# Optimization experiments

Hardware: AMD Instinct MI355X
Metric: run time of the kernel (lower is better)

## Reference

```python
import jax, jax.numpy as jnp
import numpy as np

CHUNK = 64          # config.memory_chunk_size
MAX_LR = 0.2        # config.max_memory_lr
MIN_DECAY = 0.5     # config.min_memory_decay
MAX_NORM = 30.0     # config.memory_max_norm
NORM_EPS = 1e-5     # config.norm_eps (F.normalize eps)


def setup_inputs() -> dict:
    key = jax.random.key(0)
    k0, k1 = jax.random.split(key)
    B, S, d_in, d_out = 8, 8192, 384, 384
    x = jax.random.normal(k0, (B, S, d_in), dtype=jnp.float32)
    # xavier_uniform with gain=0.1
    bound = 0.1 * float(np.sqrt(6.0 / (d_in + d_out)))
    M_init = jax.random.uniform(k1, (d_out, d_in), minval=-bound, maxval=bound, dtype=jnp.float32)
    eta_raw = jnp.asarray(np.log(0.08 / 0.92), jnp.float32)    # inv_sigmoid(memory_lr_init)
    alpha_raw = jnp.asarray(np.log(0.85 / 0.15), jnp.float32)  # inv_sigmoid(memory_decay_init)
    gate_w = jnp.zeros((1, d_in), jnp.float32)                 # nn.init.zeros_
    gate_b = jnp.full((1,), 2.0, jnp.float32)                  # nn.init.constant_(2.0)
    return {"x": x, "M_init": M_init, "eta_raw": eta_raw, "alpha_raw": alpha_raw,
            "gate_w": gate_w, "gate_b": gate_b}


def reference(x, M_init, eta_raw, alpha_raw, gate_w, gate_b):
    B, S, d_in = x.shape
    d_out = M_init.shape[0]
    eta = jax.nn.sigmoid(eta_raw) * MAX_LR
    alpha = MIN_DECAY + jax.nn.sigmoid(alpha_raw) * (1.0 - MIN_DECAY)

    n_chunks = S // CHUNK  # S chosen divisible by CHUNK => chunk_scale == 1.0
    xc = x.reshape(B, n_chunks, CHUNK, d_in).transpose(1, 0, 2, 3)  # [n,B,C,d_in]
    M0 = jnp.broadcast_to(M_init[None], (B, d_out, d_in)).astype(x.dtype)

    def step(M, chunk):
        # retrieve: queries @ M^T -> [B,C,d_out]
        out = jnp.einsum('bcd,bod->bco', chunk, M)
        # normalize keys (F.normalize: x / max(||x||, eps))
        norms = jnp.linalg.norm(chunk, axis=-1, keepdims=True)
        keys = chunk / jnp.maximum(norms, NORM_EPS)
        k_mean = keys.mean(axis=1)   # [B,d_in]
        v_mean = out.mean(axis=1)    # [B,d_out]
        # delta rule
        Mk = jnp.einsum('bod,bd->bo', M, k_mean)
        err = v_mean - Mk
        update = err[:, :, None] * k_mean[:, None, :]  # outer product [B,d_out,d_in]
        M_new = alpha * M + eta * update
        # memory gate
        gate = jax.nn.sigmoid(k_mean @ gate_w.T + gate_b)[:, :, None]  # [B,1,1]
        M_new = gate * M_new + (1.0 - gate) * M
        # frobenius norm clamp
        M_norm = jnp.linalg.norm(M_new.reshape(B, -1), axis=-1)[:, None, None]
        scale = jnp.minimum(MAX_NORM / (M_norm + 1e-6), 1.0)
        return M_new * scale, out

    M_fin, outs = jax.lax.scan(step, M0, xc)            # outs: [n,B,C,d_out]
    outputs = outs.transpose(1, 0, 2, 3).reshape(B, S, d_out)
    return outputs, M_fin
```

## Files before the change

### kernel.cpp

```cpp
#include <hip/hip_runtime.h>
#include <cmath>

#define BB 8
#define SS 8192
#define DD 384
#define CH 64
#define NC 128

typedef _Float16 h8_t __attribute__((ext_vector_type(8)));
typedef _Float16 h4_t __attribute__((ext_vector_type(4)));
typedef float f32x4 __attribute__((ext_vector_type(4)));

__global__ __launch_bounds__(512) void k1_stats(
    const float* __restrict__ x, const float* __restrict__ M0,
    const float* __restrict__ eta_raw, const float* __restrict__ alpha_raw,
    const float* __restrict__ gate_w, const float* __restrict__ gate_b,
    _Float16* __restrict__ XF, float* __restrict__ U, float* __restrict__ K32,
    _Float16* __restrict__ KF, float* __restrict__ AB, float* __restrict__ PHI2,
    _Float16* __restrict__ M0H)
{
    __shared__ float ch[CH][DD];
    __shared__ float rinv[CH];
    __shared__ float red[8];
    const int wg = blockIdx.x, tid = threadIdx.x;
    const int b = wg >> 7, n = wg & 127;
    const int lane = tid & 63, wid = tid >> 6;

    if (wg < 64) {
        for (int i = tid; i < 2304; i += 512) {
            int idx = wg * 2304 + i;
            M0H[idx] = (_Float16)M0[idx];
        }
    }
    if (tid == 0) PHI2[wg] = 0.f;

    const size_t chunk_off = (size_t)(b * SS + n * CH) * DD;
    const float4* __restrict__ xin = (const float4*)(x + chunk_off);
    h4_t* __restrict__ xf = (h4_t*)(XF + chunk_off);
    for (int i = tid; i < CH * DD / 4; i += 512) {
        float4 v = xin[i];
        int base = i * 4, r = base / DD, c = base % DD;
        ch[r][c] = v.x; ch[r][c + 1] = v.y; ch[r][c + 2] = v.z; ch[r][c + 3] = v.w;
        h4_t h; h[0] = (_Float16)v.x; h[1] = (_Float16)v.y;
        h[2] = (_Float16)v.z; h[3] = (_Float16)v.w;
        xf[i] = h;
    }
    __syncthreads();

    for (int r = wid * 8; r < wid * 8 + 8; ++r) {
        float s = 0.f;
        for (int t = 0; t < 6; ++t) { float v = ch[r][lane + 64 * t]; s += v * v; }
        for (int off = 32; off; off >>= 1) s += __shfl_xor(s, off);
        if (lane == 0) rinv[r] = 1.f / fmaxf(sqrtf(s), 1e-5f);
    }
    __syncthreads();

    float gpart = 0.f;
    for (int d = tid; d < DD; d += 512) {
        float xa = 0.f, km = 0.f;
        for (int c = 0; c < CH; ++c) { float v = ch[c][d]; xa += v; km += v * rinv[c]; }
        xa *= (1.f / 64.f); km *= (1.f / 64.f);
        int o = (b * NC + n) * DD + d;
        U[o] = xa - km; K32[o] = km; KF[o] = (_Float16)km;
        gpart += km * gate_w[d];
    }
    for (int off = 32; off; off >>= 1) gpart += __shfl_xor(gpart, off);
    if (lane == 0) red[wid] = gpart;
    __syncthreads();
    if (tid == 0) {
        float gsum = 0.f;
        for (int i = 0; i < 8; ++i) gsum += red[i];
        float g = 1.f / (1.f + expf(-(gsum + gate_b[0])));
        float eta = 0.2f / (1.f + expf(-eta_raw[0]));
        float alpha = 0.5f + 0.5f / (1.f + expf(-alpha_raw[0]));
        AB[wg * 2 + 0] = g * alpha + 1.f - g;
        AB[wg * 2 + 1] = g * eta;
    }
}

__global__ __launch_bounds__(256) void k2_rowscan(
    const float* __restrict__ M0, const float* __restrict__ U,
    const float* __restrict__ K32, const float* __restrict__ AB,
    float* __restrict__ PHI2, float* __restrict__ VT, float* __restrict__ MFW)
{
    const int b = blockIdx.x / 48, wg = blockIdx.x % 48;
    const int tid = threadIdx.x, lane = tid & 63, wid = tid >> 6;
    const int o0 = wg * 8 + wid * 2;
    float m0[6], m1[6];
    for (int t = 0; t < 6; ++t) {
        m0[t] = M0[(size_t)o0 * DD + lane + 64 * t];
        m1[t] = M0[(size_t)(o0 + 1) * DD + lane + 64 * t];
    }
    const float* __restrict__ Ub = U + (size_t)b * NC * DD;
    const float* __restrict__ Kb = K32 + (size_t)b * NC * DD;
    for (int n = 0; n < NC; ++n) {
        float u[6], kv[6];
        for (int t = 0; t < 6; ++t) {
            u[t] = Ub[n * DD + lane + 64 * t];
            kv[t] = Kb[n * DD + lane + 64 * t];
        }
        float d0 = 0.f, d1 = 0.f;
        for (int t = 0; t < 6; ++t) { d0 += m0[t] * u[t]; d1 += m1[t] * u[t]; }
        for (int off = 32; off; off >>= 1) {
            d0 += __shfl_xor(d0, off); d1 += __shfl_xor(d1, off);
        }
        float A = AB[(b * NC + n) * 2], Bc = AB[(b * NC + n) * 2 + 1];
        if (lane == 0) {
            VT[(size_t)(b * NC + n) * DD + o0] = d0;
            VT[(size_t)(b * NC + n) * DD + o0 + 1] = d1;
        }
        float c0 = Bc * d0, c1 = Bc * d1, p = 0.f;
        for (int t = 0; t < 6; ++t) {
            m0[t] = A * m0[t] + c0 * kv[t];
            m1[t] = A * m1[t] + c1 * kv[t];
            p += m0[t] * m0[t] + m1[t] * m1[t];
        }
        for (int off = 32; off; off >>= 1) p += __shfl_xor(p, off);
        if (lane == 0) atomicAdd(&PHI2[b * NC + n], p);
    }
    for (int t = 0; t < 6; ++t) {
        MFW[((size_t)b * DD + o0) * DD + lane + 64 * t] = m0[t];
        MFW[((size_t)b * DD + o0 + 1) * DD + lane + 64 * t] = m1[t];
    }
}

__global__ __launch_bounds__(256) void k3_scan(
    const float* __restrict__ AB, const float* __restrict__ PHI2,
    const float* __restrict__ VT, float* __restrict__ SIG,
    float* __restrict__ FRHO, _Float16* __restrict__ WT)
{
    const int b = blockIdx.x, tid = threadIdx.x;
    __shared__ float sA[NC], sB[NC], sP[NC], tau[NC], sig[NC];
    for (int i = tid; i < NC; i += 256) {
        sA[i] = AB[(b * NC + i) * 2];
        sB[i] = AB[(b * NC + i) * 2 + 1];
        sP[i] = PHI2[b * NC + i];
    }
    __syncthreads();
    if (tid == 0) {
        float kap = 1.f, rho = 1.f;
        for (int i = 0; i < NC; ++i) {
            float kap1 = kap * sA[i];
            sig[i] = rho * kap;
            tau[i] = sB[i] / kap1;
            float s = fminf(30.f / (rho * sqrtf(sP[i]) + 1e-6f), 1.f);
            rho *= s; kap = kap1;
        }
        FRHO[b] = rho;
    }
    __syncthreads();
    for (int i = tid; i < NC; i += 256) SIG[b * NC + i] = sig[i];
    for (int i = tid; i < NC * DD; i += 256) {
        int j = i / DD, o = i - j * DD;
        WT[((size_t)b * DD + o) * NC + j] =
            (_Float16)(tau[j] * VT[(size_t)(b * NC + j) * DD + o]);
    }
}

__global__ __launch_bounds__(256) void k4_out(
    const _Float16* __restrict__ XF, const _Float16* __restrict__ M0H,
    const _Float16* __restrict__ KF, const _Float16* __restrict__ WT,
    const float* __restrict__ SIG, const float* __restrict__ FRHO,
    const float* __restrict__ MFW, float* __restrict__ out)
{
    if (blockIdx.x >= BB * NC) {
        const int w = blockIdx.x - BB * NC;
        const float4* __restrict__ src = (const float4*)MFW;
        float4* __restrict__ dst = (float4*)(out + (size_t)BB * SS * DD);
        const int per = (BB * DD * DD / 4) / 64;
        for (int i = threadIdx.x; i < per; i += 256) {
            int idx = w * per + i;
            int b = (idx * 4) / (DD * DD);
            float r = FRHO[b];
            float4 v = src[idx];
            v.x *= r; v.y *= r; v.z *= r; v.w *= r;
            dst[idx] = v;
        }
        return;
    }
    const int b = blockIdx.x >> 7, n = blockIdx.x & 127;
    __shared__ _Float16 lds[CH * 392];
    const int tid = threadIdx.x, lane = tid & 63, w = tid >> 6;
    const int q = lane >> 4, l15 = lane & 15;

    const size_t chunk_off = (size_t)(b * SS + n * CH) * DD;
    {
        const h4_t* __restrict__ xs = (const h4_t*)(XF + chunk_off);
        for (int i = tid; i < CH * DD / 4; i += 256) {
            int base = i * 4, r = base / DD, c = base % DD;
            *(h4_t*)&lds[r * 392 + c] = xs[i];
        }
    }
    __syncthreads();

    f32x4 acc[4][6];
    for (int mi = 0; mi < 4; ++mi)
        for (int nj = 0; nj < 6; ++nj) acc[mi][nj] = (f32x4){0.f, 0.f, 0.f, 0.f};

    for (int kd = 0; kd < 12; ++kd) {
        h8_t af[4];
        for (int mi = 0; mi < 4; ++mi)
            af[mi] = *(const h8_t*)&lds[(mi * 16 + l15) * 392 + kd * 32 + q * 8];
        h8_t bf[6];
        for (int nj = 0; nj < 6; ++nj) {
            int o = w * 96 + nj * 16 + l15;
            bf[nj] = *(const h8_t*)&M0H[(size_t)o * DD + kd * 32 + q * 8];
        }
        for (int mi = 0; mi < 4; ++mi)
            for (int nj = 0; nj < 6; ++nj)
                acc[mi][nj] = __builtin_amdgcn_mfma_f32_16x16x32_f16(
                    af[mi], bf[nj], acc[mi][nj], 0, 0, 0);
    }

    const int nb = (n + 31) >> 5;
    const bool sact = (w * 32 < n);
    f32x4 sacc[4][2];
    if (sact) {
        for (int mi = 0; mi < 4; ++mi)
            for (int nj = 0; nj < 2; ++nj) sacc[mi][nj] = (f32x4){0.f, 0.f, 0.f, 0.f};
        for (int kd = 0; kd < 12; ++kd) {
            h8_t af[4];
            for (int mi = 0; mi < 4; ++mi)
                af[mi] = *(const h8_t*)&lds[(mi * 16 + l15) * 392 + kd * 32 + q * 8];
            h8_t bf[2];
            for (int nj = 0; nj < 2; ++nj) {
                int j = w * 32 + nj * 16 + l15;
                bf[nj] = *(const h8_t*)&KF[((size_t)(b * NC) + j) * DD + kd * 32 + q * 8];
            }
            for (int mi = 0; mi < 4; ++mi)
                for (int nj = 0; nj < 2; ++nj)
                    sacc[mi][nj] = __builtin_amdgcn_mfma_f32_16x16x32_f16(
                        af[mi], bf[nj], sacc[mi][nj], 0, 0, 0);
        }
    }
    __syncthreads();
    if (sact) {
        for (int mi = 0; mi < 4; ++mi)
            for (int nj = 0; nj < 2; ++nj)
                for (int r = 0; r < 4; ++r) {
                    int c = mi * 16 + q * 4 + r, j = w * 32 + nj * 16 + l15;
                    lds[c * 136 + j] = (_Float16)((j < n) ? sacc[mi][nj][r] : 0.f);
                }
    }
    __syncthreads();

    for (int kb = 0; kb < nb; ++kb) {
        h8_t af[4];
        for (int mi = 0; mi < 4; ++mi)
            af[mi] = *(const h8_t*)&lds[(mi * 16 + l15) * 136 + kb * 32 + q * 8];
        h8_t bf[6];
        for (int nj = 0; nj < 6; ++nj) {
            int o = w * 96 + nj * 16 + l15;
            bf[nj] = *(const h8_t*)&WT[((size_t)(b * DD) + o) * NC + kb * 32 + q * 8];
        }
        for (int mi = 0; mi < 4; ++mi)
            for (int nj = 0; nj < 6; ++nj)
                acc[mi][nj] = __builtin_amdgcn_mfma_f32_16x16x32_f16(
                    af[mi], bf[nj], acc[mi][nj], 0, 0, 0);
    }

    const float sg = SIG[b * NC + n];
    for (int mi = 0; mi < 4; ++mi)
        for (int nj = 0; nj < 6; ++nj)
            for (int r = 0; r < 4; ++r) {
                int c = mi * 16 + q * 4 + r, o = w * 96 + nj * 16 + l15;
                out[chunk_off + (size_t)c * DD + o] = sg * acc[mi][nj][r];
            }
}

extern "C" void kernel_launch(void* const* d_in, const int* in_sizes, int n_in,
                              void* d_out, int out_size, void* d_ws, size_t ws_size,
                              hipStream_t stream) {
    (void)in_sizes; (void)n_in; (void)out_size; (void)ws_size;
    const float* x         = (const float*)d_in[0];
    const float* M0        = (const float*)d_in[1];
    const float* eta_raw   = (const float*)d_in[2];
    const float* alpha_raw = (const float*)d_in[3];
    const float* gate_w    = (const float*)d_in[4];
    const float* gate_b    = (const float*)d_in[5];
    float* out = (float*)d_out;
    char* ws = (char*)d_ws;

    _Float16* XF  = (_Float16*)(ws);
    float*    U   = (float*)(ws + 50331648);
    float*    K32 = (float*)(ws + 51904512);
    _Float16* KF  = (_Float16*)(ws + 53477376);
    float*    AB  = (float*)(ws + 54263808);
    float*    PHI2= (float*)(ws + 54272000);
    float*    VT  = (float*)(ws + 54276096);
    float*    SIG = (float*)(ws + 55848960);
    float*    FRHO= (float*)(ws + 55853056);
    _Float16* WT  = (_Float16*)(ws + 55853312);
    float*    MFW = (float*)(ws + 56639744);
    _Float16* M0H = (_Float16*)(ws + 61358336);

    k1_stats<<<dim3(BB * NC), dim3(512), 0, stream>>>(
        x, M0, eta_raw, alpha_raw, gate_w, gate_b, XF, U, K32, KF, AB, PHI2, M0H);
    k2_rowscan<<<dim3(BB * 48), dim3(256), 0, stream>>>(
        M0, U, K32, AB, PHI2, VT, MFW);
    k3_scan<<<dim3(BB), dim3(256), 0, stream>>>(AB, PHI2, VT, SIG, FRHO, WT);
    k4_out<<<dim3(BB * NC + 64), dim3(256), 0, stream>>>(
        XF, M0H, KF, WT, SIG, FRHO, MFW, out);
}
```

Baseline: 605.5 us.

## Replace serial row-scan recurrence with Gram-matrix MFMA formulation of memory updates

Removes the 128-step sequential per-row recurrence over the memory matrix. Instead it precomputes key–key and key–u Gram matrices scaled by tau, obtains per-chunk values as V0 plus two triangular correction products, and recovers the Frobenius-norm scalars through an algebraic recurrence on sums. The final memory state becomes M0 plus a rank-128 MFMA product. Intermediates move to fp16. The two-step correction truncates the exact triangular solve and fp16 adds rounding, so accuracy depends on how small the Gram terms are. The pipeline also gains several small, low-occupancy launches.

Result: faster. 492.4 us (-18.7%).

```diff
diff --git a/kernel.cpp b/kernel.cpp
--- a/kernel.cpp
+++ b/kernel.cpp
@@ -11,17 +11,19 @@
 typedef _Float16 h4_t __attribute__((ext_vector_type(4)));
 typedef float f32x4 __attribute__((ext_vector_type(4)));
 
+#define MFMA __builtin_amdgcn_mfma_f32_16x16x32_f16
+
 __global__ __launch_bounds__(512) void k1_stats(
     const float* __restrict__ x, const float* __restrict__ M0,
     const float* __restrict__ eta_raw, const float* __restrict__ alpha_raw,
     const float* __restrict__ gate_w, const float* __restrict__ gate_b,
-    _Float16* __restrict__ XF, float* __restrict__ U, float* __restrict__ K32,
-    _Float16* __restrict__ KF, float* __restrict__ AB, float* __restrict__ PHI2,
-    _Float16* __restrict__ M0H)
+    _Float16* __restrict__ XF, _Float16* __restrict__ UF,
+    _Float16* __restrict__ KF, float* __restrict__ AB, float* __restrict__ TAB,
+    float* __restrict__ SKK, _Float16* __restrict__ M0H)
 {
     __shared__ float ch[CH][DD];
     __shared__ float rinv[CH];
-    __shared__ float red[8];
+    __shared__ float redg[8], redk[8];
     const int wg = blockIdx.x, tid = threadIdx.x;
     const int b = wg >> 7, n = wg & 127;
     const int lane = tid & 63, wid = tid >> 6;
@@ -32,7 +34,6 @@
             M0H[idx] = (_Float16)M0[idx];
         }
     }
-    if (tid == 0) PHI2[wg] = 0.f;
 
     const size_t chunk_off = (size_t)(b * SS + n * CH) * DD;
     const float4* __restrict__ xin = (const float4*)(x + chunk_off);
@@ -55,133 +56,328 @@
     }
     __syncthreads();
 
-    float gpart = 0.f;
+    float gpart = 0.f, skkp = 0.f;
     for (int d = tid; d < DD; d += 512) {
         float xa = 0.f, km = 0.f;
         for (int c = 0; c < CH; ++c) { float v = ch[c][d]; xa += v; km += v * rinv[c]; }
         xa *= (1.f / 64.f); km *= (1.f / 64.f);
         int o = (b * NC + n) * DD + d;
-        U[o] = xa - km; K32[o] = km; KF[o] = (_Float16)km;
+        UF[o] = (_Float16)(xa - km);
+        KF[o] = (_Float16)km;
         gpart += km * gate_w[d];
-    }
-    for (int off = 32; off; off >>= 1) gpart += __shfl_xor(gpart, off);
-    if (lane == 0) red[wid] = gpart;
+        skkp += km * km;
+    }
+    for (int off = 32; off; off >>= 1) {
+        gpart += __shfl_xor(gpart, off);
+        skkp += __shfl_xor(skkp, off);
+    }
+    if (lane == 0) { redg[wid] = gpart; redk[wid] = skkp; }
     __syncthreads();
     if (tid == 0) {
-        float gsum = 0.f;
-        for (int i = 0; i < 8; ++i) gsum += red[i];
+        float gsum = 0.f, ks = 0.f;
+        for (int i = 0; i < 8; ++i) { gsum += redg[i]; ks += redk[i]; }
         float g = 1.f / (1.f + expf(-(gsum + gate_b[0])));
         float eta = 0.2f / (1.f + expf(-eta_raw[0]));
         float alpha = 0.5f + 0.5f / (1.f + expf(-alpha_raw[0]));
-        AB[wg * 2 + 0] = g * alpha + 1.f - g;
-        AB[wg * 2 + 1] = g * eta;
-    }
-}
-
-__global__ __launch_bounds__(256) void k2_rowscan(
-    const float* __restrict__ M0, const float* __restrict__ U,
-    const float* __restrict__ K32, const float* __restrict__ AB,
-    float* __restrict__ PHI2, float* __restrict__ VT, float* __restrict__ MFW)
-{
-    const int b = blockIdx.x / 48, wg = blockIdx.x % 48;
-    const int tid = threadIdx.x, lane = tid & 63, wid = tid >> 6;
-    const int o0 = wg * 8 + wid * 2;
-    float m0[6], m1[6];
-    for (int t = 0; t < 6; ++t) {
-        m0[t] = M0[(size_t)o0 * DD + lane + 64 * t];
-        m1[t] = M0[(size_t)(o0 + 1) * DD + lane + 64 * t];
-    }
-    const float* __restrict__ Ub = U + (size_t)b * NC * DD;
-    const float* __restrict__ Kb = K32 + (size_t)b * NC * DD;
-    for (int n = 0; n < NC; ++n) {
-        float u[6], kv[6];
-        for (int t = 0; t < 6; ++t) {
-            u[t] = Ub[n * DD + lane + 64 * t];
-            kv[t] = Kb[n * DD + lane + 64 * t];
-        }
-        float d0 = 0.f, d1 = 0.f;
-        for (int t = 0; t < 6; ++t) { d0 += m0[t] * u[t]; d1 += m1[t] * u[t]; }
-        for (int off = 32; off; off >>= 1) {
-            d0 += __shfl_xor(d0, off); d1 += __shfl_xor(d1, off);
-        }
-        float A = AB[(b * NC + n) * 2], Bc = AB[(b * NC + n) * 2 + 1];
-        if (lane == 0) {
-            VT[(size_t)(b * NC + n) * DD + o0] = d0;
-            VT[(size_t)(b * NC + n) * DD + o0 + 1] = d1;
-        }
-        float c0 = Bc * d0, c1 = Bc * d1, p = 0.f;
-        for (int t = 0; t < 6; ++t) {
-            m0[t] = A * m0[t] + c0 * kv[t];
-            m1[t] = A * m1[t] + c1 * kv[t];
-            p += m0[t] * m0[t] + m1[t] * m1[t];
-        }
-        for (int off = 32; off; off >>= 1) p += __shfl_xor(p, off);
-        if (lane == 0) atomicAdd(&PHI2[b * NC + n], p);
-    }
-    for (int t = 0; t < 6; ++t) {
-        MFW[((size_t)b * DD + o0) * DD + lane + 64 * t] = m0[t];
-        MFW[((size_t)b * DD + o0 + 1) * DD + lane + 64 * t] = m1[t];
-    }
-}
-
-__global__ __launch_bounds__(256) void k3_scan(
-    const float* __restrict__ AB, const float* __restrict__ PHI2,
-    const float* __restrict__ VT, float* __restrict__ SIG,
-    float* __restrict__ FRHO, _Float16* __restrict__ WT)
+        float A = g * alpha + 1.f - g;
+        float Bc = g * eta;
+        AB[wg * 2 + 0] = A;
+        AB[wg * 2 + 1] = Bc;
+        TAB[wg] = Bc / A;
+        SKK[wg] = ks;
+    }
+}
+
+__global__ __launch_bounds__(256) void k_gram(
+    const _Float16* __restrict__ KF, const _Float16* __restrict__ UF,
+    const float* __restrict__ TAB, _Float16* __restrict__ GT,
+    _Float16* __restrict__ HT)
+{
+    const int b = blockIdx.x;
+    const int tid = threadIdx.x, lane = tid & 63, w = tid >> 6;
+    const int q = lane >> 4, l15 = lane & 15;
+    const _Float16* Kb = KF + (size_t)b * NC * DD;
+    const _Float16* Ub = UF + (size_t)b * NC * DD;
+    for (int pass = 0; pass < 2; ++pass) {
+        const _Float16* Bm = pass ? Kb : Ub;
+        _Float16* Out = pass ? HT : GT;
+        f32x4 acc[2][8];
+        for (int mt = 0; mt < 2; ++mt)
+            for (int nt = 0; nt < 8; ++nt) acc[mt][nt] = (f32x4){0.f, 0.f, 0.f, 0.f};
+        for (int kd = 0; kd < 12; ++kd) {
+            h8_t af[2];
+            for (int mt = 0; mt < 2; ++mt) {
+                int j = w * 32 + mt * 16 + l15;
+                af[mt] = *(const h8_t*)&Kb[(size_t)j * DD + kd * 32 + q * 8];
+            }
+            h8_t bf[8];
+            for (int nt = 0; nt < 8; ++nt) {
+                int nn = nt * 16 + l15;
+                bf[nt] = *(const h8_t*)&Bm[(size_t)nn * DD + kd * 32 + q * 8];
+            }
+            for (int mt = 0; mt < 2; ++mt)
+                for (int nt = 0; nt < 8; ++nt)
+                    acc[mt][nt] = MFMA(af[mt], bf[nt], acc[mt][nt], 0, 0, 0);
+        }
+        for (int mt = 0; mt < 2; ++mt)
+            for (int nt = 0; nt < 8; ++nt)
+                for (int r = 0; r < 4; ++r) {
+                    int j = w * 32 + mt * 16 + q * 4 + r;
+                    int nn = nt * 16 + l15;
+                    float v = (j < nn) ? TAB[b * NC + j] * acc[mt][nt][r] : 0.f;
+                    Out[((size_t)b * NC + nn) * NC + j] = (_Float16)v;
+                }
+    }
+}
+
+__global__ __launch_bounds__(256) void k_v0(
+    const _Float16* __restrict__ UF, const _Float16* __restrict__ M0H,
+    _Float16* __restrict__ V0T)
+{
+    const int b = blockIdx.x / 3, ob = blockIdx.x % 3;
+    const int tid = threadIdx.x, lane = tid & 63, w = tid >> 6;
+    const int q = lane >> 4, l15 = lane & 15;
+    f32x4 acc[2][8];
+    for (int mt = 0; mt < 2; ++mt)
+        for (int ot = 0; ot < 8; ++ot) acc[mt][ot] = (f32x4){0.f, 0.f, 0.f, 0.f};
+    for (int kd = 0; kd < 12; ++kd) {
+        h8_t af[2];
+        for (int mt = 0; mt < 2; ++mt) {
+            int n = w * 32 + mt * 16 + l15;
+            af[mt] = *(const h8_t*)&UF[((size_t)b * NC + n) * DD + kd * 32 + q * 8];
+        }
+        h8_t bf[8];
+        for (int ot = 0; ot < 8; ++ot) {
+            int o = ob * 128 + ot * 16 + l15;
+            bf[ot] = *(const h8_t*)&M0H[(size_t)o * DD + kd * 32 + q * 8];
+        }
+        for (int mt = 0; mt < 2; ++mt)
+            for (int ot = 0; ot < 8; ++ot)
+                acc[mt][ot] = MFMA(af[mt], bf[ot], acc[mt][ot], 0, 0, 0);
+    }
+    for (int mt = 0; mt < 2; ++mt)
+        for (int ot = 0; ot < 8; ++ot)
+            for (int r = 0; r < 4; ++r) {
+                int n = w * 32 + mt * 16 + q * 4 + r;
+                int o = ob * 128 + ot * 16 + l15;
+                V0T[((size_t)b * NC + n) * DD + o] = (_Float16)acc[mt][ot][r];
+            }
+}
+
+__global__ __launch_bounds__(256) void k_chain(
+    const _Float16* __restrict__ SRC, const _Float16* __restrict__ V0T,
+    const _Float16* __restrict__ GT, _Float16* __restrict__ DST)
+{
+    __shared__ _Float16 T[128 * 136];
+    const int b = blockIdx.x / 3, ob = blockIdx.x % 3;
+    const int tid = threadIdx.x, lane = tid & 63, w = tid >> 6;
+    const int q = lane >> 4, l15 = lane & 15;
+    for (int p = 0; p < 8; ++p) {
+        int j = p * 16 + (tid >> 4), o0 = (tid & 15) * 8;
+        h8_t v = *(const h8_t*)&SRC[((size_t)b * NC + j) * DD + ob * 128 + o0];
+        for (int i = 0; i < 8; ++i) T[(o0 + i) * 136 + j] = v[i];
+    }
+    __syncthreads();
+    f32x4 acc[2][8];
+    for (int mt = 0; mt < 2; ++mt)
+        for (int ot = 0; ot < 8; ++ot) acc[mt][ot] = (f32x4){0.f, 0.f, 0.f, 0.f};
+    for (int kd = 0; kd < 4; ++kd) {
+        h8_t af[2];
+        for (int mt = 0; mt < 2; ++mt) {
+            int n = w * 32 + mt * 16 + l15;
+            af[mt] = *(const h8_t*)&GT[((size_t)b * NC + n) * NC + kd * 32 + q * 8];
+        }
+        h8_t bf[8];
+        for (int ot = 0; ot < 8; ++ot)
+            bf[ot] = *(const h8_t*)&T[(ot * 16 + l15) * 136 + kd * 32 + q * 8];
+        for (int mt = 0; mt < 2; ++mt)
+            for (int ot = 0; ot < 8; ++ot)
+                acc[mt][ot] = MFMA(af[mt], bf[ot], acc[mt][ot], 0, 0, 0);
+    }
+    for (int mt = 0; mt < 2; ++mt)
+        for (int ot = 0; ot < 8; ++ot)
+            for (int r = 0; r < 4; ++r) {
+                int n = w * 32 + mt * 16 + q * 4 + r;
+                int o = ob * 128 + ot * 16 + l15;
+                size_t ix = ((size_t)b * NC + n) * DD + o;
+                DST[ix] = (_Float16)((float)V0T[ix] + acc[mt][ot][r]);
+            }
+}
+
+__global__ __launch_bounds__(256) void k_what(
+    const _Float16* __restrict__ KF, const _Float16* __restrict__ M0H,
+    const _Float16* __restrict__ HT, const _Float16* __restrict__ VHT,
+    float* __restrict__ SVP, float* __restrict__ SVVP)
+{
+    __shared__ _Float16 T[128 * 136];
+    const int b = blockIdx.x / 3, ob = blockIdx.x % 3;
+    const int tid = threadIdx.x, lane = tid & 63, w = tid >> 6;
+    const int q = lane >> 4, l15 = lane & 15;
+    for (int p = 0; p < 8; ++p) {
+        int j = p * 16 + (tid >> 4), o0 = (tid & 15) * 8;
+        h8_t v = *(const h8_t*)&VHT[((size_t)b * NC + j) * DD + ob * 128 + o0];
+        for (int i = 0; i < 8; ++i) T[(o0 + i) * 136 + j] = v[i];
+    }
+    __syncthreads();
+    f32x4 acc[2][8];
+    for (int mt = 0; mt < 2; ++mt)
+        for (int ot = 0; ot < 8; ++ot) acc[mt][ot] = (f32x4){0.f, 0.f, 0.f, 0.f};
+    for (int kd = 0; kd < 12; ++kd) {
+        h8_t af[2];
+        for (int mt = 0; mt < 2; ++mt) {
+            int n = w * 32 + mt * 16 + l15;
+            af[mt] = *(const h8_t*)&KF[((size_t)b * NC + n) * DD + kd * 32 + q * 8];
+        }
+        h8_t bf[8];
+        for (int ot = 0; ot < 8; ++ot) {
+            int o = ob * 128 + ot * 16 + l15;
+            bf[ot] = *(const h8_t*)&M0H[(size_t)o * DD + kd * 32 + q * 8];
+        }
+        for (int mt = 0; mt < 2; ++mt)
+            for (int ot = 0; ot < 8; ++ot)
+                acc[mt][ot] = MFMA(af[mt], bf[ot], acc[mt][ot], 0, 0, 0);
+    }
+    for (int kd = 0; kd < 4; ++kd) {
+        h8_t af[2];
+        for (int mt = 0; mt < 2; ++mt) {
+            int n = w * 32 + mt * 16 + l15;
+            af[mt] = *(const h8_t*)&HT[((size_t)b * NC + n) * NC + kd * 32 + q * 8];
+        }
+        h8_t bf[8];
+        for (int ot = 0; ot < 8; ++ot)
+            bf[ot] = *(const h8_t*)&T[(ot * 16 + l15) * 136 + kd * 32 + q * 8];
+        for (int mt = 0; mt < 2; ++mt)
+            for (int ot = 0; ot < 8; ++ot)
+                acc[mt][ot] = MFMA(af[mt], bf[ot], acc[mt][ot], 0, 0, 0);
+    }
+    for (int mt = 0; mt < 2; ++mt)
+        for (int r = 0; r < 4; ++r) {
+            int n = w * 32 + mt * 16 + q * 4 + r;
+            float sv = 0.f, svv = 0.f;
+            for (int ot = 0; ot < 8; ++ot) {
+                float vh = (float)T[(ot * 16 + l15) * 136 + n];
+                sv += acc[mt][ot][r] * vh;
+                svv += vh * vh;
+            }
+            sv += __shfl_xor(sv, 1); svv += __shfl_xor(svv, 1);
+            sv += __shfl_xor(sv, 2); svv += __shfl_xor(svv, 2);
+            sv += __shfl_xor(sv, 4); svv += __shfl_xor(svv, 4);
+            sv += __shfl_xor(sv, 8); svv += __shfl_xor(svv, 8);
+            if (l15 == 0) {
+                SVP[(b * 3 + ob) * NC + n] = sv;
+                SVVP[(b * 3 + ob) * NC + n] = svv;
+            }
+        }
+}
+
+__global__ __launch_bounds__(256) void k_scalar(
+    const float* __restrict__ M0, const float* __restrict__ AB,
+    const float* __restrict__ SKK, const float* __restrict__ SVP,
+    const float* __restrict__ SVVP, float* __restrict__ SIG,
+    float* __restrict__ FRHO)
 {
     const int b = blockIdx.x, tid = threadIdx.x;
-    __shared__ float sA[NC], sB[NC], sP[NC], tau[NC], sig[NC];
-    for (int i = tid; i < NC; i += 256) {
-        sA[i] = AB[(b * NC + i) * 2];
-        sB[i] = AB[(b * NC + i) * 2 + 1];
-        sP[i] = PHI2[b * NC + i];
-    }
+    __shared__ float red[4];
+    __shared__ float sig_s[NC];
+    float p = 0.f;
+    const float4* m4 = (const float4*)M0;
+    for (int i = tid; i < DD * DD / 4; i += 256) {
+        float4 v = m4[i];
+        p += v.x * v.x + v.y * v.y + v.z * v.z + v.w * v.w;
+    }
+    for (int off = 32; off; off >>= 1) p += __shfl_xor(p, off);
+    if ((tid & 63) == 0) red[tid >> 6] = p;
     __syncthreads();
     if (tid == 0) {
-        float kap = 1.f, rho = 1.f;
-        for (int i = 0; i < NC; ++i) {
-            float kap1 = kap * sA[i];
-            sig[i] = rho * kap;
-            tau[i] = sB[i] / kap1;
-            float s = fminf(30.f / (rho * sqrtf(sP[i]) + 1e-6f), 1.f);
-            rho *= s; kap = kap1;
-        }
-        FRHO[b] = rho;
-    }
-    __syncthreads();
-    for (int i = tid; i < NC; i += 256) SIG[b * NC + i] = sig[i];
-    for (int i = tid; i < NC * DD; i += 256) {
-        int j = i / DD, o = i - j * DD;
-        WT[((size_t)b * DD + o) * NC + j] =
-            (_Float16)(tau[j] * VT[(size_t)(b * NC + j) * DD + o]);
+        float phi2 = red[0] + red[1] + red[2] + red[3];
+        float an = 1.f, rho = 1.f;
+        for (int n = 0; n < NC; ++n) {
+            float A = AB[(b * NC + n) * 2], Bc = AB[(b * NC + n) * 2 + 1];
+            sig_s[n] = rho * an;
+            float a2 = an * an;
+            float sv = a2 * (SVP[(b * 3 + 0) * NC + n] + SVP[(b * 3 + 1) * NC + n]
+                             + SVP[(b * 3 + 2) * NC + n]);
+            float svv = a2 * (SVVP[(b * 3 + 0) * NC + n] + SVVP[(b * 3 + 1) * NC + n]
+                              + SVVP[(b * 3 + 2) * NC + n]);
+            phi2 = A * A * phi2 + 2.f * A * Bc * sv + Bc * Bc * svv * SKK[b * NC + n];
+            float s = fminf(30.f / (rho * sqrtf(phi2) + 1e-6f), 1.f);
+            rho *= s; an *= A;
+        }
+        FRHO[b] = rho * an;
+    }
+    __syncthreads();
+    for (int i = tid; i < NC; i += 256) SIG[b * NC + i] = sig_s[i];
+}
+
+__global__ __launch_bounds__(256) void k_trans(
+    const _Float16* __restrict__ VHT, const _Float16* __restrict__ KF,
+    const float* __restrict__ TAB, _Float16* __restrict__ WTH,
+    _Float16* __restrict__ KFT)
+{
+    __shared__ _Float16 T[128 * 72];
+    const int b = blockIdx.x / 6, ob = blockIdx.x % 6, tid = threadIdx.x;
+    for (int pass = 0; pass < 2; ++pass) {
+        const _Float16* Src = pass ? KF : VHT;
+        _Float16* Dst = pass ? KFT : WTH;
+        if (pass) __syncthreads();
+        for (int pp = 0; pp < 4; ++pp) {
+            int j = pp * 32 + (tid >> 3), oo = (tid & 7) * 8;
+            *(h8_t*)&T[j * 72 + oo] =
+                *(const h8_t*)&Src[((size_t)b * NC + j) * DD + ob * 64 + oo];
+        }
+        __syncthreads();
+        for (int c = 0; c < 4; ++c) {
+            int idx = c * 256 + tid;
+            int ol = idx >> 4, jc = (idx & 15) * 8;
+            h8_t v;
+            for (int i = 0; i < 8; ++i) {
+                float t = (float)T[(jc + i) * 72 + ol];
+                if (!pass) t *= TAB[b * NC + jc + i];
+                v[i] = (_Float16)t;
+            }
+            *(h8_t*)&Dst[((size_t)b * DD + ob * 64 + ol) * NC + jc] = v;
+        }
     }
 }
 
 __global__ __launch_bounds__(256) void k4_out(
     const _Float16* __restrict__ XF, const _Float16* __restrict__ M0H,
-    const _Float16* __restrict__ KF, const _Float16* __restrict__ WT,
-    const float* __restrict__ SIG, const float* __restrict__ FRHO,
-    const float* __restrict__ MFW, float* __restrict__ out)
-{
+    const _Float16* __restrict__ KF, const _Float16* __restrict__ WTH,
+    const _Float16* __restrict__ KFT, const float* __restrict__ SIG,
+    const float* __restrict__ FRHO, const float* __restrict__ M0,
+    float* __restrict__ out)
+{
+    const int tid = threadIdx.x, lane = tid & 63, w = tid >> 6;
+    const int q = lane >> 4, l15 = lane & 15;
+
     if (blockIdx.x >= BB * NC) {
-        const int w = blockIdx.x - BB * NC;
-        const float4* __restrict__ src = (const float4*)MFW;
-        float4* __restrict__ dst = (float4*)(out + (size_t)BB * SS * DD);
-        const int per = (BB * DD * DD / 4) / 64;
-        for (int i = threadIdx.x; i < per; i += 256) {
-            int idx = w * per + i;
-            int b = (idx * 4) / (DD * DD);
-            float r = FRHO[b];
-            float4 v = src[idx];
-            v.x *= r; v.y *= r; v.z *= r; v.w *= r;
-            dst[idx] = v;
-        }
+        const int tw = blockIdx.x - BB * NC;
+        const int b = tw / 12, sub = tw % 12;
+        const int obk = sub >> 1, dh = sub & 1;
+        const int o_t = obk * 64 + w * 16;
+        f32x4 acc[12];
+        for (int dt = 0; dt < 12; ++dt) acc[dt] = (f32x4){0.f, 0.f, 0.f, 0.f};
+        for (int kd = 0; kd < 4; ++kd) {
+            h8_t af = *(const h8_t*)&WTH[((size_t)b * DD + o_t + l15) * NC + kd * 32 + q * 8];
+            for (int dt = 0; dt < 12; ++dt) {
+                int d = dh * 192 + dt * 16 + l15;
+                h8_t bf = *(const h8_t*)&KFT[((size_t)b * DD + d) * NC + kd * 32 + q * 8];
+                acc[dt] = MFMA(af, bf, acc[dt], 0, 0, 0);
+            }
+        }
+        float fr = FRHO[b];
+        float* dst = out + (size_t)BB * SS * DD;
+        for (int dt = 0; dt < 12; ++dt)
+            for (int r = 0; r < 4; ++r) {
+                int o = o_t + q * 4 + r, d = dh * 192 + dt * 16 + l15;
+                dst[((size_t)b * DD + o) * DD + d] =
+                    fr * (M0[(size_t)o * DD + d] + acc[dt][r]);
+            }
         return;
     }
+
     const int b = blockIdx.x >> 7, n = blockIdx.x & 127;
     __shared__ _Float16 lds[CH * 392];
-    const int tid = threadIdx.x, lane = tid & 63, w = tid >> 6;
-    const int q = lane >> 4, l15 = lane & 15;
 
     const size_t chunk_off = (size_t)(b * SS + n * CH) * DD;
     {
@@ -208,8 +404,7 @@
         }
         for (int mi = 0; mi < 4; ++mi)
             for (int nj = 0; nj < 6; ++nj)
-                acc[mi][nj] = __builtin_amdgcn_mfma_f32_16x16x32_f16(
-                    af[mi], bf[nj], acc[mi][nj], 0, 0, 0);
+                acc[mi][nj] = MFMA(af[mi], bf[nj], acc[mi][nj], 0, 0, 0);
     }
 
     const int nb = (n + 31) >> 5;
@@ -229,8 +424,7 @@
             }
             for (int mi = 0; mi < 4; ++mi)
                 for (int nj = 0; nj < 2; ++nj)
-                    sacc[mi][nj] = __builtin_amdgcn_mfma_f32_16x16x32_f16(
-                        af[mi], bf[nj], sacc[mi][nj], 0, 0, 0);
+                    sacc[mi][nj] = MFMA(af[mi], bf[nj], sacc[mi][nj], 0, 0, 0);
         }
     }
     __syncthreads();
@@ -251,12 +445,11 @@
         h8_t bf[6];
         for (int nj = 0; nj < 6; ++nj) {
             int o = w * 96 + nj * 16 + l15;
-            bf[nj] = *(const h8_t*)&WT[((size_t)(b * DD) + o) * NC + kb * 32 + q * 8];
+            bf[nj] = *(const h8_t*)&WTH[((size_t)(b * DD) + o) * NC + kb * 32 + q * 8];
         }
         for (int mi = 0; mi < 4; ++mi)
             for (int nj = 0; nj < 6; ++nj)
-                acc[mi][nj] = __builtin_amdgcn_mfma_f32_16x16x32_f16(
-                    af[mi], bf[nj], acc[mi][nj], 0, 0, 0);
+                acc[mi][nj] = MFMA(af[mi], bf[nj], acc[mi][nj], 0, 0, 0);
     }
 
     const float sg = SIG[b * NC + n];
@@ -282,23 +475,33 @@
     char* ws = (char*)d_ws;
 
     _Float16* XF  = (_Float16*)(ws);
-    float*    U   = (float*)(ws + 50331648);
-    float*    K32 = (float*)(ws + 51904512);
-    _Float16* KF  = (_Float16*)(ws + 53477376);
-    float*    AB  = (float*)(ws + 54263808);
-    float*    PHI2= (float*)(ws + 54272000);
-    float*    VT  = (float*)(ws + 54276096);
-    float*    SIG = (float*)(ws + 55848960);
-    float*    FRHO= (float*)(ws + 55853056);
-    _Float16* WT  = (_Float16*)(ws + 55853312);
-    float*    MFW = (float*)(ws + 56639744);
-    _Float16* M0H = (_Float16*)(ws + 61358336);
+    _Float16* UF  = (_Float16*)(ws + 50331648);
+    _Float16* KF  = (_Float16*)(ws + 51118080);
+    _Float16* M0H = (_Float16*)(ws + 51904512);
+    _Float16* GT  = (_Float16*)(ws + 52199424);
+    _Float16* HT  = (_Float16*)(ws + 52461568);
+    _Float16* V0T = (_Float16*)(ws + 52723712);
+    _Float16* VTA = (_Float16*)(ws + 53510144);
+    _Float16* VTB = (_Float16*)(ws + 54296576);
+    _Float16* WTH = (_Float16*)(ws + 55083008);
+    _Float16* KFT = (_Float16*)(ws + 55869440);
+    float*    AB  = (float*)(ws + 56655872);
+    float*    TAB = (float*)(ws + 56664064);
+    float*    SKK = (float*)(ws + 56668160);
+    float*    SVP = (float*)(ws + 56672256);
+    float*    SVVP= (float*)(ws + 56684544);
+    float*    SIG = (float*)(ws + 56696832);
+    float*    FRHO= (float*)(ws + 56700928);
 
     k1_stats<<<dim3(BB * NC), dim3(512), 0, stream>>>(
-        x, M0, eta_raw, alpha_raw, gate_w, gate_b, XF, U, K32, KF, AB, PHI2, M0H);
-    k2_rowscan<<<dim3(BB * 48), dim3(256), 0, stream>>>(
-        M0, U, K32, AB, PHI2, VT, MFW);
-    k3_scan<<<dim3(BB), dim3(256), 0, stream>>>(AB, PHI2, VT, SIG, FRHO, WT);
-    k4_out<<<dim3(BB * NC + 64), dim3(256), 0, stream>>>(
-        XF, M0H, KF, WT, SIG, FRHO, MFW, out);
-}
+        x, M0, eta_raw, alpha_raw, gate_w, gate_b, XF, UF, KF, AB, TAB, SKK, M0H);
+    k_gram<<<dim3(BB), dim3(256), 0, stream>>>(KF, UF, TAB, GT, HT);
+    k_v0<<<dim3(BB * 3), dim3(256), 0, stream>>>(UF, M0H, V0T);
+    k_chain<<<dim3(BB * 3), dim3(256), 0, stream>>>(V0T, V0T, GT, VTA);
+    k_chain<<<dim3(BB * 3), dim3(256), 0, stream>>>(VTA, V0T, GT, VTB);
+    k_what<<<dim3(BB * 3), dim3(256), 0, stream>>>(KF, M0H, HT, VTB, SVP, SVVP);
+    k_scalar<<<dim3(BB), dim3(256), 0, stream>>>(M0, AB, SKK, SVP, SVVP, SIG, FRHO);
+    k_trans<<<dim3(BB * 6), dim3(256), 0, stream>>>(VTB, KF, TAB, WTH, KFT);
+    k4_out<<<dim3(BB * NC + 96), dim3(256), 0, stream>>>(
+        XF, M0H, KF, WTH, KFT, SIG, FRHO, M0, out);
+}
```
